# Kernel optimization log

Measured on AMD Instinct MI355X. Metric: run time of the kernel, lower is better.

Reference implementation:

```python
import jax, jax.numpy as jnp
import numpy as np

EPS = 1e-5
B, NA, T, D, H, L, DFF, E = 4, 64, 128, 128, 8, 3, 512, 65536
NN = T * NA  # nodes per graph = t*n after reshape(b, t*n, f)
DH = D // H


def _layer_norm(x, g, b):
    m = x.mean(-1, keepdims=True)
    v = ((x - m) ** 2).mean(-1, keepdims=True)
    return (x - m) * jax.lax.rsqrt(v + EPS) * g + b


def _pos_encoding(t, d):
    pos = jnp.arange(t, dtype=jnp.float32)[:, None]
    i = jnp.arange(0, d, 2, dtype=jnp.float32)
    ang = pos * jnp.exp(-jnp.log(10000.0) * i / d)
    pe = jnp.zeros((t, d), jnp.float32)
    return pe.at[:, 0::2].set(jnp.sin(ang)).at[:, 1::2].set(jnp.cos(ang))


def _forward(all_hist_feat, edge_weight, hist_w, hist_b,
             attn_wq, attn_bq, attn_wk, attn_bk, attn_wv, attn_bv, attn_wo, attn_bo,
             ln1_g, ln1_b, ff_w1, ff_b1, ff_w2, ff_b2, ln2_g, ln2_b,
             bn_g, bn_b, lin_graph_w, lin_graph_b, edge_index):
    b, n, t, _ = all_hist_feat.shape
    # history embedding: Linear(3, D)  -> [b, n, t, D]
    x = all_hist_feat @ hist_w + hist_b
    # sinusoidal positional encoding over the time axis
    out_e = x + _pos_encoding(t, D)
    scale = 1.0 / jnp.sqrt(jnp.asarray(DH, jnp.float32))
    for l in range(L):  # small fixed layer count
        q = out_e @ attn_wq[l] + attn_bq[l]
        k = out_e @ attn_wk[l] + attn_bk[l]
        v = out_e @ attn_wv[l] + attn_bv[l]
        qh = q.reshape(b, n, t, H, DH)
        kh = k.reshape(b, n, t, H, DH)
        vh = v.reshape(b, n, t, H, DH)
        scores = jnp.einsum('bnqhd,bnkhd->bnhqk', qh, kh) * scale
        attn = jax.nn.softmax(scores, axis=-1)
        o = jnp.einsum('bnhqk,bnkhd->bnqhd', attn, vh).reshape(b, n, t, D)
        o = o @ attn_wo[l] + attn_bo[l]
        h1 = _layer_norm(out_e + o, ln1_g[l], ln1_b[l])
        ff = jax.nn.relu(h1 @ ff_w1[l] + ff_b1[l]) @ ff_w2[l] + ff_b2[l]
        out_e = _layer_norm(h1 + ff, ln2_g[l], ln2_b[l])
    # graph stage: nodes are (time, agent) pairs, index = time*n + agent
    graph_w = out_e.transpose(0, 2, 1, 3).reshape(b, t * n, D)
    graph_x = x.transpose(0, 2, 1, 3).reshape(b, t * n, D)
    # GCNConv_Fixed_W (no self loops, no normalize): per-node score then
    # edge-weighted scatter-add from source to target (PyG convention)
    s = (graph_w * graph_x).sum(-1)  # [b, t*n]
    src, dst = edge_index[:, 0], edge_index[:, 1]

    def agg(s_b, src_b, dst_b, ew_b):
        return jax.ops.segment_sum(ew_b * s_b[src_b], dst_b, num_segments=NN)

    graph_out = jax.vmap(agg)(s, src, dst, edge_weight)  # [b, t*n]
    g = graph_out.reshape(b, t, n)
    # BatchNorm2d(1) on [b, 1, n, t]: single channel -> global batch stats
    m = g.mean()
    var = g.var()
    g = (g - m) * jax.lax.rsqrt(var + EPS) * bn_g[0] + bn_b[0]
    g4 = g.transpose(0, 2, 1)[..., None]  # [b, n, t, 1]
    return g4 @ lin_graph_w + lin_graph_b  # [b, n, t, D]


def setup_inputs() -> dict:
    keys = iter(jax.random.split(jax.random.key(0), 64))

    def nrm(shape, scale):
        return jax.random.normal(next(keys), shape, jnp.float32) * scale

    inp = {
        'all_hist_feat': nrm((B, NA, T, 3), 1.0),
        'edge_index': jax.random.randint(next(keys), (B, 2, E), 0, NN, jnp.int32),
        'edge_weight': jax.random.uniform(next(keys), (B, E), jnp.float32),
        'hist_w': nrm((3, D), 0.5), 'hist_b': nrm((D,), 0.02),
        'attn_wq': nrm((L, D, D), D ** -0.5), 'attn_bq': jnp.zeros((L, D)),
        'attn_wk': nrm((L, D, D), D ** -0.5), 'attn_bk': jnp.zeros((L, D)),
        'attn_wv': nrm((L, D, D), D ** -0.5), 'attn_bv': jnp.zeros((L, D)),
        'attn_wo': nrm((L, D, D), D ** -0.5), 'attn_bo': jnp.zeros((L, D)),
        'ln1_g': jnp.ones((L, D)), 'ln1_b': jnp.zeros((L, D)),
        'ff_w1': nrm((L, D, DFF), D ** -0.5), 'ff_b1': jnp.zeros((L, DFF)),
        'ff_w2': nrm((L, DFF, D), DFF ** -0.5), 'ff_b2': jnp.zeros((L, D)),
        'ln2_g': jnp.ones((L, D)), 'ln2_b': jnp.zeros((L, D)),
        'bn_g': jnp.ones((1,)), 'bn_b': jnp.zeros((1,)),
        'lin_graph_w': nrm((1, D), 1.0), 'lin_graph_b': jnp.zeros((D,)),
    }
    return inp


def reference(all_hist_feat, edge_index, edge_weight, hist_w, hist_b,
              attn_wq, attn_bq, attn_wk, attn_bk, attn_wv, attn_bv, attn_wo, attn_bo,
              ln1_g, ln1_b, ff_w1, ff_b1, ff_w2, ff_b2, ln2_g, ln2_b,
              bn_g, bn_b, lin_graph_w, lin_graph_b):
    return _forward(all_hist_feat, edge_weight, hist_w, hist_b,
                    attn_wq, attn_bq, attn_wk, attn_bk, attn_wv, attn_bv, attn_wo, attn_bo,
                    ln1_g, ln1_b, ff_w1, ff_b1, ff_w2, ff_b2, ln2_g, ln2_b,
                    bn_g, bn_b, lin_graph_w, lin_graph_b, edge_index)
```

## Files before the change

### kernel.cpp

```cpp
#include <hip/hip_runtime.h>
#include <hip/hip_bf16.h>
#include <math.h>

#define EPS_ 1e-5f
constexpr int B_ = 4, NA = 64, T_ = 128, D_ = 128, H_ = 8, L_ = 3, DFF = 512, E_ = 65536;
constexpr int DH = D_ / H_;
constexpr int NN = T_ * NA;
constexpr int NTOT = B_ * NA * T_;
constexpr int QLD = 384;
constexpr size_t NE_ = (size_t)NTOT * D_;

typedef __bf16 bf16x8 __attribute__((ext_vector_type(8)));
typedef float f32x4 __attribute__((ext_vector_type(4)));

__global__ __launch_bounds__(256) void embed_kernel(
    const float* __restrict__ hist, const float* __restrict__ w,
    const float* __restrict__ b, float* __restrict__ x, float* __restrict__ e) {
  int idx = blockIdx.x * 256 + threadIdx.x;
  if (idx >= NTOT * D_) return;
  int d = idx & (D_ - 1);
  int r = idx >> 7;
  int t = r & (T_ - 1);
  const float* hp = hist + (size_t)r * 3;
  float acc = b[d];
  acc += hp[0] * w[0 * D_ + d];
  acc += hp[1] * w[1 * D_ + d];
  acc += hp[2] * w[2 * D_ + d];
  x[idx] = acc;
  int p = d >> 1;
  float ang = (float)t * expf(-logf(10000.f) * (2.f * (float)p) / (float)D_);
  float pe = (d & 1) ? cosf(ang) : sinf(ang);
  e[idx] = acc + pe;
}

__global__ __launch_bounds__(256) void convert_weights(
    const float* __restrict__ wq, const float* __restrict__ wk,
    const float* __restrict__ wv, const float* __restrict__ wo,
    const float* __restrict__ w1, const float* __restrict__ w2,
    __bf16* __restrict__ hi, __bf16* __restrict__ lo) {
  const int LW = 196608;
  int idx = blockIdx.x * 256 + threadIdx.x;
  if (idx >= L_ * LW) return;
  int l = idx / LW;
  int rem = idx - l * LW;
  float src;
  int n, k, K, segoff;
  if (rem < 49152) {
    n = rem >> 7; k = rem & 127; K = 128; segoff = 0;
    int which = n >> 7, nl = n & 127;
    const float* W = (which == 0) ? wq : (which == 1) ? wk : wv;
    src = W[(size_t)l * 16384 + k * 128 + nl];
  } else if (rem < 65536) {
    int r2 = rem - 49152;
    n = r2 >> 7; k = r2 & 127; K = 128; segoff = 49152;
    src = wo[(size_t)l * 16384 + k * 128 + n];
  } else if (rem < 131072) {
    int r2 = rem - 65536;
    n = r2 >> 7; k = r2 & 127; K = 128; segoff = 65536;
    src = w1[(size_t)l * 65536 + k * 512 + n];
  } else {
    int r2 = rem - 131072;
    n = r2 >> 9; k = r2 & 511; K = 512; segoff = 131072;
    src = w2[(size_t)l * 65536 + k * 128 + n];
  }
  int nt = n >> 4, kt = k >> 5;
  int lane = ((k >> 3) & 3) * 16 + (n & 15);
  int j = k & 7;
  int dst = l * LW + segoff + ((nt * (K / 32) + kt) * 64 + lane) * 8 + j;
  __bf16 h = (__bf16)src;
  hi[dst] = h;
  lo[dst] = (__bf16)(src - (float)h);
}

__global__ __launch_bounds__(256) void bias_pack(
    const float* __restrict__ bq, const float* __restrict__ bk,
    const float* __restrict__ bv, float* __restrict__ pb) {
  int idx = blockIdx.x * 256 + threadIdx.x;
  if (idx >= L_ * QLD) return;
  int l = idx / QLD, n = idx - l * QLD;
  int which = n >> 7, nl = n & 127;
  const float* src = (which == 0) ? bq : (which == 1) ? bk : bv;
  pb[idx] = src[l * 128 + nl];
}

__device__ __forceinline__ void split8(const float* __restrict__ p,
                                       bf16x8& hi, bf16x8& lo) {
  float4 x0 = *(const float4*)p;
  float4 x1 = *(const float4*)(p + 4);
  float xv[8] = {x0.x, x0.y, x0.z, x0.w, x1.x, x1.y, x1.z, x1.w};
#pragma unroll
  for (int j = 0; j < 8; ++j) {
    __bf16 h = (__bf16)xv[j];
    hi[j] = h;
    lo[j] = (__bf16)(xv[j] - (float)h);
  }
}

template <int EPI, int K>
__global__ __launch_bounds__(256) void gemm_big(
    const float* __restrict__ A, int lda,
    const __bf16* __restrict__ Whi, const __bf16* __restrict__ Wlo,
    const float* __restrict__ bias,
    float* __restrict__ C, int ldc) {
  const int wave = threadIdx.x >> 6;
  const int lane = threadIdx.x & 63;
  const int m16 = lane & 15;
  const int quad = lane >> 4;
  const int wrow = wave >> 1, wcol = wave & 1;
  const int row0 = blockIdx.y * 128 + wrow * 64;
  const int col0 = blockIdx.x * 128 + wcol * 64;
  const int ctb = col0 >> 4;

  f32x4 acc[4][4] = {};
#pragma unroll
  for (int k0 = 0; k0 < K; k0 += 32) {
    bf16x8 ahi[4], alo[4];
#pragma unroll
    for (int mf = 0; mf < 4; ++mf)
      split8(A + (size_t)(row0 + mf * 16 + m16) * lda + k0 + quad * 8, ahi[mf], alo[mf]);
    bf16x8 bhi[4], blo[4];
#pragma unroll
    for (int nf = 0; nf < 4; ++nf) {
      size_t off = ((size_t)(ctb + nf) * (K / 32) + (k0 >> 5)) * 512 + lane * 8;
      bhi[nf] = *(const bf16x8*)(Whi + off);
      blo[nf] = *(const bf16x8*)(Wlo + off);
    }
#pragma unroll
    for (int mf = 0; mf < 4; ++mf)
#pragma unroll
      for (int nf = 0; nf < 4; ++nf) {
        acc[mf][nf] = __builtin_amdgcn_mfma_f32_16x16x32_bf16(ahi[mf], bhi[nf], acc[mf][nf], 0, 0, 0);
        acc[mf][nf] = __builtin_amdgcn_mfma_f32_16x16x32_bf16(ahi[mf], blo[nf], acc[mf][nf], 0, 0, 0);
        acc[mf][nf] = __builtin_amdgcn_mfma_f32_16x16x32_bf16(alo[mf], bhi[nf], acc[mf][nf], 0, 0, 0);
      }
  }
#pragma unroll
  for (int mf = 0; mf < 4; ++mf)
#pragma unroll
    for (int nf = 0; nf < 4; ++nf) {
      int c = col0 + nf * 16 + m16;
      float bj = bias[c];
#pragma unroll
      for (int reg = 0; reg < 4; ++reg) {
        int r = row0 + mf * 16 + quad * 4 + reg;
        float v = acc[mf][nf][reg] + bj;
        if (EPI == 1) v = fmaxf(v, 0.f);
        C[(size_t)r * ldc + c] = v;
      }
    }
}

template <int K>
__global__ __launch_bounds__(256) void gemm_ln(
    const float* __restrict__ A, int lda,
    const __bf16* __restrict__ Whi, const __bf16* __restrict__ Wlo,
    const float* __restrict__ bias, const float* __restrict__ resid,
    const float* __restrict__ lng, const float* __restrict__ lnb,
    float* __restrict__ C) {
  const int wave = threadIdx.x >> 6;
  const int lane = threadIdx.x & 63;
  const int m16 = lane & 15;
  const int quad = lane >> 4;
  const int wrow = wave >> 1, wcol = wave & 1;
  const int row0 = blockIdx.y * 64 + wrow * 32;
  const int col0 = wcol * 64;
  const int ctb = wcol * 4;

  f32x4 acc[2][4] = {};
#pragma unroll
  for (int k0 = 0; k0 < K; k0 += 32) {
    bf16x8 ahi[2], alo[2];
#pragma unroll
    for (int mf = 0; mf < 2; ++mf)
      split8(A + (size_t)(row0 + mf * 16 + m16) * lda + k0 + quad * 8, ahi[mf], alo[mf]);
    bf16x8 bhi[4], blo[4];
#pragma unroll
    for (int nf = 0; nf < 4; ++nf) {
      size_t off = ((size_t)(ctb + nf) * (K / 32) + (k0 >> 5)) * 512 + lane * 8;
      bhi[nf] = *(const bf16x8*)(Whi + off);
      blo[nf] = *(const bf16x8*)(Wlo + off);
    }
#pragma unroll
    for (int mf = 0; mf < 2; ++mf)
#pragma unroll
      for (int nf = 0; nf < 4; ++nf) {
        acc[mf][nf] = __builtin_amdgcn_mfma_f32_16x16x32_bf16(ahi[mf], bhi[nf], acc[mf][nf], 0, 0, 0);
        acc[mf][nf] = __builtin_amdgcn_mfma_f32_16x16x32_bf16(ahi[mf], blo[nf], acc[mf][nf], 0, 0, 0);
        acc[mf][nf] = __builtin_amdgcn_mfma_f32_16x16x32_bf16(alo[mf], bhi[nf], acc[mf][nf], 0, 0, 0);
      }
  }
  __shared__ float rs[64][2], rq[64][2];
#pragma unroll
  for (int mf = 0; mf < 2; ++mf)
#pragma unroll
    for (int reg = 0; reg < 4; ++reg) {
      int lr = wrow * 32 + mf * 16 + quad * 4 + reg;
      int gr = blockIdx.y * 64 + lr;
      float s = 0.f, qq = 0.f;
#pragma unroll
      for (int nf = 0; nf < 4; ++nf) {
        int c = col0 + nf * 16 + m16;
        float v = acc[mf][nf][reg] + bias[c] + resid[(size_t)gr * 128 + c];
        acc[mf][nf][reg] = v;
        s += v;
        qq += v * v;
      }
#pragma unroll
      for (int off = 1; off < 16; off <<= 1) {
        s += __shfl_xor(s, off, 64);
        qq += __shfl_xor(qq, off, 64);
      }
      if (m16 == 0) { rs[lr][wcol] = s; rq[lr][wcol] = qq; }
    }
  __syncthreads();
#pragma unroll
  for (int mf = 0; mf < 2; ++mf)
#pragma unroll
    for (int reg = 0; reg < 4; ++reg) {
      int lr = wrow * 32 + mf * 16 + quad * 4 + reg;
      int gr = blockIdx.y * 64 + lr;
      float mean = (rs[lr][0] + rs[lr][1]) * (1.f / 128.f);
      float var = (rq[lr][0] + rq[lr][1]) * (1.f / 128.f) - mean * mean;
      float rstd = rsqrtf(var + EPS_);
#pragma unroll
      for (int nf = 0; nf < 4; ++nf) {
        int c = col0 + nf * 16 + m16;
        C[(size_t)gr * 128 + c] = (acc[mf][nf][reg] - mean) * rstd * lng[c] + lnb[c];
      }
    }
}

template <int SDOT>
__global__ __launch_bounds__(256) void ff2_ln(
    const float* __restrict__ A,
    const __bf16* __restrict__ Whi, const __bf16* __restrict__ Wlo,
    const float* __restrict__ bias, const float* __restrict__ resid,
    const float* __restrict__ lng, const float* __restrict__ lnb,
    float* __restrict__ C,
    const float* __restrict__ bx, float* __restrict__ sdst) {
  const int wave = threadIdx.x >> 6;
  const int lane = threadIdx.x & 63;
  const int m16 = lane & 15;
  const int quad = lane >> 4;
  const int wrow = wave >> 1, wcol = wave & 1;
  const int grow0 = blockIdx.y * 64;
  const int lrow0 = wrow * 32;
  const int col0 = wcol * 64;
  const int ctb = wcol * 4;

  __shared__ float As[64][129];

  f32x4 acc[2][4] = {};
  for (int kc = 0; kc < 4; ++kc) {
    if (kc) __syncthreads();
#pragma unroll
    for (int u = 0; u < 8; ++u) {
      int unit = threadIdx.x + u * 256;
      int r = unit >> 5, c4 = unit & 31;
      float4 v = *(const float4*)(A + (size_t)(grow0 + r) * 512 + kc * 128 + c4 * 4);
      As[r][c4 * 4 + 0] = v.x;
      As[r][c4 * 4 + 1] = v.y;
      As[r][c4 * 4 + 2] = v.z;
      As[r][c4 * 4 + 3] = v.w;
    }
    __syncthreads();
#pragma unroll
    for (int kt = 0; kt < 4; ++kt) {
      bf16x8 ahi[2], alo[2];
#pragma unroll
      for (int mf = 0; mf < 2; ++mf)
        split8(&As[lrow0 + mf * 16 + m16][kt * 32 + quad * 8], ahi[mf], alo[mf]);
      bf16x8 bhi[4], blo[4];
#pragma unroll
      for (int nf = 0; nf < 4; ++nf) {
        size_t off = ((size_t)(ctb + nf) * 16 + (kc * 4 + kt)) * 512 + lane * 8;
        bhi[nf] = *(const bf16x8*)(Whi + off);
        blo[nf] = *(const bf16x8*)(Wlo + off);
      }
#pragma unroll
      for (int mf = 0; mf < 2; ++mf)
#pragma unroll
        for (int nf = 0; nf < 4; ++nf) {
          acc[mf][nf] = __builtin_amdgcn_mfma_f32_16x16x32_bf16(ahi[mf], bhi[nf], acc[mf][nf], 0, 0, 0);
          acc[mf][nf] = __builtin_amdgcn_mfma_f32_16x16x32_bf16(ahi[mf], blo[nf], acc[mf][nf], 0, 0, 0);
          acc[mf][nf] = __builtin_amdgcn_mfma_f32_16x16x32_bf16(alo[mf], bhi[nf], acc[mf][nf], 0, 0, 0);
        }
    }
  }
  __shared__ float rs[64][2], rq[64][2];
  __shared__ float sd[64][2];
#pragma unroll
  for (int mf = 0; mf < 2; ++mf)
#pragma unroll
    for (int reg = 0; reg < 4; ++reg) {
      int lr = lrow0 + mf * 16 + quad * 4 + reg;
      int gr = grow0 + lr;
      float s = 0.f, qq = 0.f;
#pragma unroll
      for (int nf = 0; nf < 4; ++nf) {
        int c = col0 + nf * 16 + m16;
        float v = acc[mf][nf][reg] + bias[c] + resid[(size_t)gr * 128 + c];
        acc[mf][nf][reg] = v;
        s += v;
        qq += v * v;
      }
#pragma unroll
      for (int off = 1; off < 16; off <<= 1) {
        s += __shfl_xor(s, off, 64);
        qq += __shfl_xor(qq, off, 64);
      }
      if (m16 == 0) { rs[lr][wcol] = s; rq[lr][wcol] = qq; }
    }
  __syncthreads();
#pragma unroll
  for (int mf = 0; mf < 2; ++mf)
#pragma unroll
    for (int reg = 0; reg < 4; ++reg) {
      int lr = lrow0 + mf * 16 + quad * 4 + reg;
      int gr = grow0 + lr;
      float mean = (rs[lr][0] + rs[lr][1]) * (1.f / 128.f);
      float var = (rq[lr][0] + rq[lr][1]) * (1.f / 128.f) - mean * mean;
      float rstd = rsqrtf(var + EPS_);
      float sdp = 0.f;
#pragma unroll
      for (int nf = 0; nf < 4; ++nf) {
        int c = col0 + nf * 16 + m16;
        float v = (acc[mf][nf][reg] - mean) * rstd * lng[c] + lnb[c];
        C[(size_t)gr * 128 + c] = v;
        if (SDOT) sdp += v * bx[(size_t)gr * 128 + c];
      }
      if (SDOT) {
#pragma unroll
        for (int off = 1; off < 16; off <<= 1) sdp += __shfl_xor(sdp, off, 64);
        if (m16 == 0) sd[lr][wcol] = sdp;
      }
    }
  if (SDOT) {
    __syncthreads();
    if (threadIdx.x < 64) {
      int lr = threadIdx.x;
      int gr = grow0 + lr;
      float sv = sd[lr][0] + sd[lr][1];
      int t = gr & (T_ - 1);
      int bn = gr >> 7;
      int n = bn & (NA - 1);
      int b = bn >> 6;
      sdst[(size_t)b * NN + t * NA + n] = sv;
    }
  }
}

__global__ __launch_bounds__(256) void attn_mfma(float* __restrict__ qkv) {
  const int h = blockIdx.x & (H_ - 1);
  const int bn = blockIdx.x >> 3;
  const int wave = threadIdx.x >> 6;
  const int lane = threadIdx.x & 63;
  const int m16 = lane & 15;
  const int quad = lane >> 4;
  const int row0 = wave * 32;
  const float* Qb = qkv + (size_t)bn * T_ * QLD + h * DH;
  const float* Kb = Qb + 128;
  const float* Vb = Qb + 256;
  float* Ob = (float*)Vb;

  __shared__ __bf16 Plds[4][32][136];
  __shared__ __bf16 KH[8][32][8], KL[8][32][8];
  __shared__ __bf16 VH[4][64][8], VL[4][64][8];

  for (int u = threadIdx.x; u < 1024; u += 256) {
    int isV = u >> 9;
    int r2 = u & 511;
    int t = r2 >> 2, c4 = r2 & 3;
    float4 v = *(const float4*)((isV ? Vb : Kb) + (size_t)t * QLD + c4 * 4);
    float xv[4] = {v.x, v.y, v.z, v.w};
#pragma unroll
    for (int i = 0; i < 4; ++i) {
      int dh = c4 * 4 + i;
      __bf16 hh = (__bf16)xv[i];
      __bf16 ll = (__bf16)(xv[i] - (float)hh);
      if (isV) {
        int kc = t >> 5, rem = t & 31;
        int vl = (rem >> 3) * 16 + dh;
        VH[kc][vl][rem & 7] = hh;
        VL[kc][vl][rem & 7] = ll;
      } else {
        int nf = t >> 4;
        int kl = (dh >> 3) * 16 + (t & 15);
        KH[nf][kl][dh & 7] = hh;
        KL[nf][kl][dh & 7] = ll;
      }
    }
  }

  bf16x8 qhi[2], qlo[2];
#pragma unroll
  for (int mf = 0; mf < 2; ++mf) {
    if (quad < 2) {
      split8(Qb + (size_t)(row0 + mf * 16 + m16) * QLD + quad * 8, qhi[mf], qlo[mf]);
    } else {
#pragma unroll
      for (int j = 0; j < 8; ++j) { qhi[mf][j] = (__bf16)0.f; qlo[mf][j] = (__bf16)0.f; }
    }
  }
  __syncthreads();

  f32x4 acc[2][8] = {};
#pragma unroll
  for (int nf = 0; nf < 8; ++nf) {
    bf16x8 khi, klo;
    if (quad < 2) {
      khi = *(const bf16x8*)&KH[nf][lane][0];
      klo = *(const bf16x8*)&KL[nf][lane][0];
    } else {
#pragma unroll
      for (int j = 0; j < 8; ++j) { khi[j] = (__bf16)0.f; klo[j] = (__bf16)0.f; }
    }
#pragma unroll
    for (int mf = 0; mf < 2; ++mf) {
      acc[mf][nf] = __builtin_amdgcn_mfma_f32_16x16x32_bf16(qhi[mf], khi, acc[mf][nf], 0, 0, 0);
      acc[mf][nf] = __builtin_amdgcn_mfma_f32_16x16x32_bf16(qhi[mf], klo, acc[mf][nf], 0, 0, 0);
      acc[mf][nf] = __builtin_amdgcn_mfma_f32_16x16x32_bf16(qlo[mf], khi, acc[mf][nf], 0, 0, 0);
    }
  }

  const float scale = 0.25f;
#pragma unroll
  for (int mf = 0; mf < 2; ++mf)
#pragma unroll
    for (int reg = 0; reg < 4; ++reg) {
      float mx = -1e30f;
#pragma unroll
      for (int nf = 0; nf < 8; ++nf) mx = fmaxf(mx, acc[mf][nf][reg]);
#pragma unroll
      for (int off = 1; off < 16; off <<= 1) mx = fmaxf(mx, __shfl_xor(mx, off, 64));
      float sum = 0.f;
#pragma unroll
      for (int nf = 0; nf < 8; ++nf) {
        float e = __expf((acc[mf][nf][reg] - mx) * scale);
        acc[mf][nf][reg] = e;
        sum += e;
      }
#pragma unroll
      for (int off = 1; off < 16; off <<= 1) sum += __shfl_xor(sum, off, 64);
      float inv = 1.f / sum;
#pragma unroll
      for (int nf = 0; nf < 8; ++nf) acc[mf][nf][reg] *= inv;
    }

#pragma unroll
  for (int mf = 0; mf < 2; ++mf)
#pragma unroll
    for (int nf = 0; nf < 8; ++nf)
#pragma unroll
      for (int reg = 0; reg < 4; ++reg)
        Plds[wave][mf * 16 + quad * 4 + reg][nf * 16 + m16] = (__bf16)acc[mf][nf][reg];

  f32x4 oacc[2] = {};
#pragma unroll
  for (int kc = 0; kc < 4; ++kc) {
    bf16x8 pa0 = *(const bf16x8*)&Plds[wave][m16][kc * 32 + quad * 8];
    bf16x8 pa1 = *(const bf16x8*)&Plds[wave][16 + m16][kc * 32 + quad * 8];
    bf16x8 vhi = *(const bf16x8*)&VH[kc][lane][0];
    bf16x8 vlo = *(const bf16x8*)&VL[kc][lane][0];
    oacc[0] = __builtin_amdgcn_mfma_f32_16x16x32_bf16(pa0, vhi, oacc[0], 0, 0, 0);
    oacc[0] = __builtin_amdgcn_mfma_f32_16x16x32_bf16(pa0, vlo, oacc[0], 0, 0, 0);
    oacc[1] = __builtin_amdgcn_mfma_f32_16x16x32_bf16(pa1, vhi, oacc[1], 0, 0, 0);
    oacc[1] = __builtin_amdgcn_mfma_f32_16x16x32_bf16(pa1, vlo, oacc[1], 0, 0, 0);
  }

#pragma unroll
  for (int mf = 0; mf < 2; ++mf)
#pragma unroll
    for (int reg = 0; reg < 4; ++reg) {
      int r = row0 + mf * 16 + quad * 4 + reg;
      Ob[(size_t)r * QLD + m16] = oacc[mf][reg];
    }
}

__global__ __launch_bounds__(256) void scatter_kernel(
    const float* __restrict__ s, const int* __restrict__ ei,
    const float* __restrict__ ew, float* __restrict__ g) {
  int idx = blockIdx.x * 256 + threadIdx.x;
  if (idx >= B_ * E_) return;
  int b = idx >> 16;
  int e = idx & (E_ - 1);
  int src = ei[(size_t)b * 2 * E_ + e];
  int dst = ei[(size_t)b * 2 * E_ + E_ + e];
  float w = ew[(size_t)b * E_ + e];
  atomicAdd(&g[(size_t)b * NN + dst], w * s[(size_t)b * NN + src]);
}

__global__ __launch_bounds__(256) void stats_partial(
    const float* __restrict__ g, float* __restrict__ st) {
  int i = blockIdx.x * 256 + threadIdx.x;
  float v = g[i];
  float sum = v, sq = v * v;
#pragma unroll
  for (int off = 32; off; off >>= 1) {
    sum += __shfl_down(sum, off, 64);
    sq += __shfl_down(sq, off, 64);
  }
  __shared__ float s1[4], s2[4];
  int w = threadIdx.x >> 6;
  if ((threadIdx.x & 63) == 0) { s1[w] = sum; s2[w] = sq; }
  __syncthreads();
  if (threadIdx.x == 0) {
    atomicAdd(&st[0], s1[0] + s1[1] + s1[2] + s1[3]);
    atomicAdd(&st[1], s2[0] + s2[1] + s2[2] + s2[3]);
  }
}

__global__ __launch_bounds__(256) void final_kernel(
    const float* __restrict__ g, const float* __restrict__ st,
    const float* __restrict__ bng, const float* __restrict__ bnb,
    const float* __restrict__ lw, const float* __restrict__ lb,
    float* __restrict__ out) {
  int idx = blockIdx.x * 256 + threadIdx.x;
  if (idx >= NTOT * D_) return;
  int d = idx & (D_ - 1);
  int r = idx >> 7;
  int t = r & (T_ - 1);
  int bn = r >> 7;
  int n = bn & (NA - 1);
  int b = bn >> 6;
  const float invn = 1.f / (float)(B_ * NN);
  float m = st[0] * invn;
  float var = st[1] * invn - m * m;
  float rs = rsqrtf(var + EPS_);
  float gv = g[(size_t)b * NN + t * NA + n];
  float val = (gv - m) * rs * bng[0] + bnb[0];
  out[idx] = val * lw[d] + lb[d];
}

extern "C" void kernel_launch(void* const* d_in, const int* in_sizes, int n_in,
                              void* d_out, int out_size, void* d_ws, size_t ws_size,
                              hipStream_t stream) {
  const float* hist = (const float*)d_in[0];
  const int* eidx = (const int*)d_in[1];
  const float* ew = (const float*)d_in[2];
  const float* hw = (const float*)d_in[3];
  const float* hb = (const float*)d_in[4];
  const float* wq = (const float*)d_in[5];
  const float* bq = (const float*)d_in[6];
  const float* wk = (const float*)d_in[7];
  const float* bk = (const float*)d_in[8];
  const float* wv = (const float*)d_in[9];
  const float* bv = (const float*)d_in[10];
  const float* wo = (const float*)d_in[11];
  const float* bo = (const float*)d_in[12];
  const float* ln1g = (const float*)d_in[13];
  const float* ln1b = (const float*)d_in[14];
  const float* w1 = (const float*)d_in[15];
  const float* b1 = (const float*)d_in[16];
  const float* w2 = (const float*)d_in[17];
  const float* b2 = (const float*)d_in[18];
  const float* ln2g = (const float*)d_in[19];
  const float* ln2b = (const float*)d_in[20];
  const float* bng = (const float*)d_in[21];
  const float* bnb = (const float*)d_in[22];
  const float* lgw = (const float*)d_in[23];
  const float* lgb = (const float*)d_in[24];
  float* out = (float*)d_out;

  float* ws = (float*)d_ws;
  const size_t NE = NE_;
  float* bx = ws + 0 * NE;
  float* be = ws + 1 * NE;
  float* h1 = ws + 2 * NE;
  float* qkv = ws + 3 * NE;
  float* ffmid = ws + 3 * NE;
  float* bs_ = ws + 7 * NE;
  float* bg_ = bs_ + NTOT;
  float* bst = bg_ + NTOT;
  float* pbias = bst + 2;
  const int LW = 196608;
  __bf16* whiB = (__bf16*)(pbias + L_ * QLD);
  __bf16* wloB = whiB + (size_t)L_ * LW;

  convert_weights<<<(L_ * LW + 255) / 256, 256, 0, stream>>>(
      wq, wk, wv, wo, w1, w2, whiB, wloB);
  bias_pack<<<(L_ * QLD + 255) / 256, 256, 0, stream>>>(bq, bk, bv, pbias);
  embed_kernel<<<(NTOT * D_) / 256, 256, 0, stream>>>(hist, hw, hb, bx, be);

  for (int l = 0; l < L_; ++l) {
    const __bf16* hiL = whiB + (size_t)l * LW;
    const __bf16* loL = wloB + (size_t)l * LW;
    gemm_big<0, 128><<<dim3(3, NTOT / 128), 256, 0, stream>>>(
        be, 128, hiL, loL, pbias + l * QLD, qkv, QLD);
    attn_mfma<<<B_ * NA * H_, 256, 0, stream>>>(qkv);
    gemm_ln<128><<<dim3(1, NTOT / 64), 256, 0, stream>>>(
        qkv + 256, QLD, hiL + 49152, loL + 49152, bo + l * D_, be,
        ln1g + l * D_, ln1b + l * D_, h1);
    gemm_big<1, 128><<<dim3(4, NTOT / 128), 256, 0, stream>>>(
        h1, 128, hiL + 65536, loL + 65536, b1 + l * DFF, ffmid, 512);
    if (l < L_ - 1) {
      ff2_ln<0><<<dim3(1, NTOT / 64), 256, 0, stream>>>(
          ffmid, hiL + 131072, loL + 131072, b2 + l * D_, h1,
          ln2g + l * D_, ln2b + l * D_, be, nullptr, nullptr);
    } else {
      ff2_ln<1><<<dim3(1, NTOT / 64), 256, 0, stream>>>(
          ffmid, hiL + 131072, loL + 131072, b2 + l * D_, h1,
          ln2g + l * D_, ln2b + l * D_, be, bx, bs_);
    }
  }

  hipMemsetAsync(bg_, 0, ((size_t)B_ * NN + 2) * sizeof(float), stream);
  scatter_kernel<<<(B_ * E_) / 256, 256, 0, stream>>>(bs_, eidx, ew, bg_);
  stats_partial<<<(B_ * NN) / 256, 256, 0, stream>>>(bg_, bst);
  final_kernel<<<(NTOT * D_) / 256, 256, 0, stream>>>(bg_, bst, bng, bnb, lgw, lgb, out);
}
```

Measured before the change: 538.9 us.

## Fuse FFN up-projection, ReLU and down-projection+LayerNorm into one kernel

```diff
diff --git a/kernel.cpp b/kernel.cpp
--- a/kernel.cpp
+++ b/kernel.cpp
@@ -231,76 +231,93 @@
 }
 
 template <int SDOT>
-__global__ __launch_bounds__(256) void ff2_ln(
+__global__ __launch_bounds__(256) void ff_fused(
     const float* __restrict__ A,
-    const __bf16* __restrict__ Whi, const __bf16* __restrict__ Wlo,
-    const float* __restrict__ bias, const float* __restrict__ resid,
+    const __bf16* __restrict__ W1hi, const __bf16* __restrict__ W1lo,
+    const float* __restrict__ b1v,
+    const __bf16* __restrict__ W2hi, const __bf16* __restrict__ W2lo,
+    const float* __restrict__ b2v, const float* __restrict__ resid,
     const float* __restrict__ lng, const float* __restrict__ lnb,
     float* __restrict__ C,
     const float* __restrict__ bx, float* __restrict__ sdst) {
+  extern __shared__ float Amid[];
   const int wave = threadIdx.x >> 6;
   const int lane = threadIdx.x & 63;
   const int m16 = lane & 15;
   const int quad = lane >> 4;
-  const int wrow = wave >> 1, wcol = wave & 1;
-  const int grow0 = blockIdx.y * 64;
-  const int lrow0 = wrow * 32;
-  const int col0 = wcol * 64;
-  const int ctb = wcol * 4;
-
-  __shared__ float As[64][129];
-
-  f32x4 acc[2][4] = {};
-  for (int kc = 0; kc < 4; ++kc) {
-    if (kc) __syncthreads();
-#pragma unroll
-    for (int u = 0; u < 8; ++u) {
-      int unit = threadIdx.x + u * 256;
-      int r = unit >> 5, c4 = unit & 31;
-      float4 v = *(const float4*)(A + (size_t)(grow0 + r) * 512 + kc * 128 + c4 * 4);
-      As[r][c4 * 4 + 0] = v.x;
-      As[r][c4 * 4 + 1] = v.y;
-      As[r][c4 * 4 + 2] = v.z;
-      As[r][c4 * 4 + 3] = v.w;
-    }
-    __syncthreads();
+  const int grow0 = blockIdx.x * 32;
+
+  {
+    f32x4 acc[2][8] = {};
 #pragma unroll
     for (int kt = 0; kt < 4; ++kt) {
       bf16x8 ahi[2], alo[2];
 #pragma unroll
       for (int mf = 0; mf < 2; ++mf)
-        split8(&As[lrow0 + mf * 16 + m16][kt * 32 + quad * 8], ahi[mf], alo[mf]);
-      bf16x8 bhi[4], blo[4];
-#pragma unroll
-      for (int nf = 0; nf < 4; ++nf) {
-        size_t off = ((size_t)(ctb + nf) * 16 + (kc * 4 + kt)) * 512 + lane * 8;
-        bhi[nf] = *(const bf16x8*)(Whi + off);
-        blo[nf] = *(const bf16x8*)(Wlo + off);
-      }
-#pragma unroll
-      for (int mf = 0; mf < 2; ++mf)
-#pragma unroll
-        for (int nf = 0; nf < 4; ++nf) {
-          acc[mf][nf] = __builtin_amdgcn_mfma_f32_16x16x32_bf16(ahi[mf], bhi[nf], acc[mf][nf], 0, 0, 0);
-          acc[mf][nf] = __builtin_amdgcn_mfma_f32_16x16x32_bf16(ahi[mf], blo[nf], acc[mf][nf], 0, 0, 0);
-          acc[mf][nf] = __builtin_amdgcn_mfma_f32_16x16x32_bf16(alo[mf], bhi[nf], acc[mf][nf], 0, 0, 0);
+        split8(A + (size_t)(grow0 + mf * 16 + m16) * 128 + kt * 32 + quad * 8, ahi[mf], alo[mf]);
+#pragma unroll
+      for (int nf = 0; nf < 8; ++nf) {
+        size_t off = ((size_t)(wave * 8 + nf) * 4 + kt) * 512 + lane * 8;
+        bf16x8 bhi = *(const bf16x8*)(W1hi + off);
+        bf16x8 blo = *(const bf16x8*)(W1lo + off);
+#pragma unroll
+        for (int mf = 0; mf < 2; ++mf) {
+          acc[mf][nf] = __builtin_amdgcn_mfma_f32_16x16x32_bf16(ahi[mf], bhi, acc[mf][nf], 0, 0, 0);
+          acc[mf][nf] = __builtin_amdgcn_mfma_f32_16x16x32_bf16(ahi[mf], blo, acc[mf][nf], 0, 0, 0);
+          acc[mf][nf] = __builtin_amdgcn_mfma_f32_16x16x32_bf16(alo[mf], bhi, acc[mf][nf], 0, 0, 0);
         }
-    }
-  }
-  __shared__ float rs[64][2], rq[64][2];
-  __shared__ float sd[64][2];
+      }
+    }
+#pragma unroll
+    for (int mf = 0; mf < 2; ++mf)
+#pragma unroll
+      for (int nf = 0; nf < 8; ++nf) {
+        int c = wave * 128 + nf * 16 + m16;
+        float bj = b1v[c];
+#pragma unroll
+        for (int reg = 0; reg < 4; ++reg) {
+          int r = mf * 16 + quad * 4 + reg;
+          Amid[r * 513 + c] = fmaxf(acc[mf][nf][reg] + bj, 0.f);
+        }
+      }
+  }
+  __syncthreads();
+
+  f32x4 acc2[2][2] = {};
+#pragma unroll
+  for (int kt = 0; kt < 16; ++kt) {
+    bf16x8 ahi[2], alo[2];
+#pragma unroll
+    for (int mf = 0; mf < 2; ++mf)
+      split8(&Amid[(mf * 16 + m16) * 513 + kt * 32 + quad * 8], ahi[mf], alo[mf]);
+#pragma unroll
+    for (int nf = 0; nf < 2; ++nf) {
+      size_t off = ((size_t)(wave * 2 + nf) * 16 + kt) * 512 + lane * 8;
+      bf16x8 bhi = *(const bf16x8*)(W2hi + off);
+      bf16x8 blo = *(const bf16x8*)(W2lo + off);
+#pragma unroll
+      for (int mf = 0; mf < 2; ++mf) {
+        acc2[mf][nf] = __builtin_amdgcn_mfma_f32_16x16x32_bf16(ahi[mf], bhi, acc2[mf][nf], 0, 0, 0);
+        acc2[mf][nf] = __builtin_amdgcn_mfma_f32_16x16x32_bf16(ahi[mf], blo, acc2[mf][nf], 0, 0, 0);
+        acc2[mf][nf] = __builtin_amdgcn_mfma_f32_16x16x32_bf16(alo[mf], bhi, acc2[mf][nf], 0, 0, 0);
+      }
+    }
+  }
+
+  __shared__ float rs[32][4], rq[32][4], sd[32][4];
+  const int col0 = wave * 32;
 #pragma unroll
   for (int mf = 0; mf < 2; ++mf)
 #pragma unroll
     for (int reg = 0; reg < 4; ++reg) {
-      int lr = lrow0 + mf * 16 + quad * 4 + reg;
+      int lr = mf * 16 + quad * 4 + reg;
       int gr = grow0 + lr;
       float s = 0.f, qq = 0.f;
 #pragma unroll
-      for (int nf = 0; nf < 4; ++nf) {
+      for (int nf = 0; nf < 2; ++nf) {
         int c = col0 + nf * 16 + m16;
-        float v = acc[mf][nf][reg] + bias[c] + resid[(size_t)gr * 128 + c];
-        acc[mf][nf][reg] = v;
+        float v = acc2[mf][nf][reg] + b2v[c] + resid[(size_t)gr * 128 + c];
+        acc2[mf][nf][reg] = v;
         s += v;
         qq += v * v;
       }
@@ -309,38 +326,38 @@
         s += __shfl_xor(s, off, 64);
         qq += __shfl_xor(qq, off, 64);
       }
-      if (m16 == 0) { rs[lr][wcol] = s; rq[lr][wcol] = qq; }
+      if (m16 == 0) { rs[lr][wave] = s; rq[lr][wave] = qq; }
     }
   __syncthreads();
 #pragma unroll
   for (int mf = 0; mf < 2; ++mf)
 #pragma unroll
     for (int reg = 0; reg < 4; ++reg) {
-      int lr = lrow0 + mf * 16 + quad * 4 + reg;
+      int lr = mf * 16 + quad * 4 + reg;
       int gr = grow0 + lr;
-      float mean = (rs[lr][0] + rs[lr][1]) * (1.f / 128.f);
-      float var = (rq[lr][0] + rq[lr][1]) * (1.f / 128.f) - mean * mean;
+      float mean = (rs[lr][0] + rs[lr][1] + rs[lr][2] + rs[lr][3]) * (1.f / 128.f);
+      float var = (rq[lr][0] + rq[lr][1] + rq[lr][2] + rq[lr][3]) * (1.f / 128.f) - mean * mean;
       float rstd = rsqrtf(var + EPS_);
       float sdp = 0.f;
 #pragma unroll
-      for (int nf = 0; nf < 4; ++nf) {
+      for (int nf = 0; nf < 2; ++nf) {
         int c = col0 + nf * 16 + m16;
-        float v = (acc[mf][nf][reg] - mean) * rstd * lng[c] + lnb[c];
+        float v = (acc2[mf][nf][reg] - mean) * rstd * lng[c] + lnb[c];
         C[(size_t)gr * 128 + c] = v;
         if (SDOT) sdp += v * bx[(size_t)gr * 128 + c];
       }
       if (SDOT) {
 #pragma unroll
         for (int off = 1; off < 16; off <<= 1) sdp += __shfl_xor(sdp, off, 64);
-        if (m16 == 0) sd[lr][wcol] = sdp;
+        if (m16 == 0) sd[lr][wave] = sdp;
       }
     }
   if (SDOT) {
     __syncthreads();
-    if (threadIdx.x < 64) {
+    if (threadIdx.x < 32) {
       int lr = threadIdx.x;
       int gr = grow0 + lr;
-      float sv = sd[lr][0] + sd[lr][1];
+      float sv = sd[lr][0] + sd[lr][1] + sd[lr][2] + sd[lr][3];
       int t = gr & (T_ - 1);
       int bn = gr >> 7;
       int n = bn & (NA - 1);
@@ -568,7 +585,6 @@
   float* be = ws + 1 * NE;
   float* h1 = ws + 2 * NE;
   float* qkv = ws + 3 * NE;
-  float* ffmid = ws + 3 * NE;
   float* bs_ = ws + 7 * NE;
   float* bg_ = bs_ + NTOT;
   float* bst = bg_ + NTOT;
@@ -576,6 +592,16 @@
   const int LW = 196608;
   __bf16* whiB = (__bf16*)(pbias + L_ * QLD);
   __bf16* wloB = whiB + (size_t)L_ * LW;
+
+  const size_t ffshm = (size_t)32 * 513 * sizeof(float);
+  static bool ff_attr_done = false;
+  if (!ff_attr_done) {
+    (void)hipFuncSetAttribute(reinterpret_cast<const void*>(&ff_fused<0>),
+                              hipFuncAttributeMaxDynamicSharedMemorySize, (int)ffshm);
+    (void)hipFuncSetAttribute(reinterpret_cast<const void*>(&ff_fused<1>),
+                              hipFuncAttributeMaxDynamicSharedMemorySize, (int)ffshm);
+    ff_attr_done = true;
+  }
 
   convert_weights<<<(L_ * LW + 255) / 256, 256, 0, stream>>>(
       wq, wk, wv, wo, w1, w2, whiB, wloB);
@@ -591,15 +617,15 @@
     gemm_ln<128><<<dim3(1, NTOT / 64), 256, 0, stream>>>(
         qkv + 256, QLD, hiL + 49152, loL + 49152, bo + l * D_, be,
         ln1g + l * D_, ln1b + l * D_, h1);
-    gemm_big<1, 128><<<dim3(4, NTOT / 128), 256, 0, stream>>>(
-        h1, 128, hiL + 65536, loL + 65536, b1 + l * DFF, ffmid, 512);
     if (l < L_ - 1) {
-      ff2_ln<0><<<dim3(1, NTOT / 64), 256, 0, stream>>>(
-          ffmid, hiL + 131072, loL + 131072, b2 + l * D_, h1,
+      ff_fused<0><<<NTOT / 32, 256, ffshm, stream>>>(
+          h1, hiL + 65536, loL + 65536, b1 + l * DFF,
+          hiL + 131072, loL + 131072, b2 + l * D_, h1,
           ln2g + l * D_, ln2b + l * D_, be, nullptr, nullptr);
     } else {
-      ff2_ln<1><<<dim3(1, NTOT / 64), 256, 0, stream>>>(
-          ffmid, hiL + 131072, loL + 131072, b2 + l * D_, h1,
+      ff_fused<1><<<NTOT / 32, 256, ffshm, stream>>>(
+          h1, hiL + 65536, loL + 65536, b1 + l * DFF,
+          hiL + 131072, loL + 131072, b2 + l * D_, h1,
           ln2g + l * D_, ln2b + l * D_, be, bx, bs_);
     }
   }
```

New measurement: 547.3 us. About the same (+1.6%).

## Fuse QKV projection into attention kernel per (batch,agent,head) block

Applied to the files above, without the earlier changes.

```diff
diff --git a/kernel.cpp b/kernel.cpp
--- a/kernel.cpp
+++ b/kernel.cpp
@@ -350,7 +350,11 @@
   }
 }
 
-__global__ __launch_bounds__(256) void attn_mfma(float* __restrict__ qkv) {
+__global__ __launch_bounds__(256) void attn_fused(
+    const float* __restrict__ A,
+    const __bf16* __restrict__ Whi, const __bf16* __restrict__ Wlo,
+    const float* __restrict__ pb,
+    float* __restrict__ O) {
   const int h = blockIdx.x & (H_ - 1);
   const int bn = blockIdx.x >> 3;
   const int wave = threadIdx.x >> 6;
@@ -358,45 +362,78 @@
   const int m16 = lane & 15;
   const int quad = lane >> 4;
   const int row0 = wave * 32;
-  const float* Qb = qkv + (size_t)bn * T_ * QLD + h * DH;
-  const float* Kb = Qb + 128;
-  const float* Vb = Qb + 256;
-  float* Ob = (float*)Vb;
+  const float* Ab = A + (size_t)bn * T_ * 128;
 
   __shared__ __bf16 Plds[4][32][136];
   __shared__ __bf16 KH[8][32][8], KL[8][32][8];
   __shared__ __bf16 VH[4][64][8], VL[4][64][8];
-
-  for (int u = threadIdx.x; u < 1024; u += 256) {
-    int isV = u >> 9;
-    int r2 = u & 511;
-    int t = r2 >> 2, c4 = r2 & 3;
-    float4 v = *(const float4*)((isV ? Vb : Kb) + (size_t)t * QLD + c4 * 4);
-    float xv[4] = {v.x, v.y, v.z, v.w};
-#pragma unroll
-    for (int i = 0; i < 4; ++i) {
-      int dh = c4 * 4 + i;
-      __bf16 hh = (__bf16)xv[i];
-      __bf16 ll = (__bf16)(xv[i] - (float)hh);
-      if (isV) {
+  __bf16* QHw = &Plds[wave][0][0];
+  __bf16* QLw = QHw + 512;
+
+  f32x4 qkv[2][3] = {};
+#pragma unroll
+  for (int k0 = 0; k0 < 128; k0 += 32) {
+    bf16x8 ahi[2], alo[2];
+#pragma unroll
+    for (int mf = 0; mf < 2; ++mf)
+      split8(Ab + (size_t)(row0 + mf * 16 + m16) * 128 + k0 + quad * 8, ahi[mf], alo[mf]);
+    bf16x8 bhi[3], blo[3];
+#pragma unroll
+    for (int s = 0; s < 3; ++s) {
+      size_t off = ((size_t)(s * 8 + h) * 4 + (k0 >> 5)) * 512 + lane * 8;
+      bhi[s] = *(const bf16x8*)(Whi + off);
+      blo[s] = *(const bf16x8*)(Wlo + off);
+    }
+#pragma unroll
+    for (int mf = 0; mf < 2; ++mf)
+#pragma unroll
+      for (int s = 0; s < 3; ++s) {
+        qkv[mf][s] = __builtin_amdgcn_mfma_f32_16x16x32_bf16(ahi[mf], bhi[s], qkv[mf][s], 0, 0, 0);
+        qkv[mf][s] = __builtin_amdgcn_mfma_f32_16x16x32_bf16(ahi[mf], blo[s], qkv[mf][s], 0, 0, 0);
+        qkv[mf][s] = __builtin_amdgcn_mfma_f32_16x16x32_bf16(alo[mf], bhi[s], qkv[mf][s], 0, 0, 0);
+      }
+  }
+
+#pragma unroll
+  for (int mf = 0; mf < 2; ++mf)
+#pragma unroll
+    for (int reg = 0; reg < 4; ++reg) {
+      const int tl = mf * 16 + quad * 4 + reg;
+      const int t = row0 + tl;
+      const int dh = m16;
+      {
+        float v = qkv[mf][0][reg] + pb[h * 16 + dh];
+        __bf16 hh = (__bf16)v;
+        __bf16 ll = (__bf16)(v - (float)hh);
+        int idx = mf * 256 + ((dh >> 3) * 16 + (tl & 15)) * 8 + (dh & 7);
+        QHw[idx] = hh;
+        QLw[idx] = ll;
+      }
+      {
+        float v = qkv[mf][1][reg] + pb[128 + h * 16 + dh];
+        __bf16 hh = (__bf16)v;
+        __bf16 ll = (__bf16)(v - (float)hh);
+        KH[t >> 4][(dh >> 3) * 16 + (t & 15)][dh & 7] = hh;
+        KL[t >> 4][(dh >> 3) * 16 + (t & 15)][dh & 7] = ll;
+      }
+      {
+        float v = qkv[mf][2][reg] + pb[256 + h * 16 + dh];
+        __bf16 hh = (__bf16)v;
+        __bf16 ll = (__bf16)(v - (float)hh);
         int kc = t >> 5, rem = t & 31;
         int vl = (rem >> 3) * 16 + dh;
         VH[kc][vl][rem & 7] = hh;
         VL[kc][vl][rem & 7] = ll;
-      } else {
-        int nf = t >> 4;
-        int kl = (dh >> 3) * 16 + (t & 15);
-        KH[nf][kl][dh & 7] = hh;
-        KL[nf][kl][dh & 7] = ll;
-      }
-    }
-  }
+      }
+    }
 
   bf16x8 qhi[2], qlo[2];
 #pragma unroll
   for (int mf = 0; mf < 2; ++mf) {
     if (quad < 2) {
-      split8(Qb + (size_t)(row0 + mf * 16 + m16) * QLD + quad * 8, qhi[mf], qlo[mf]);
+      int idx = mf * 256 + (quad * 16 + m16) * 8;
+      qhi[mf] = *(const bf16x8*)&QHw[idx];
+      qlo[mf] = *(const bf16x8*)&QLw[idx];
     } else {
 #pragma unroll
       for (int j = 0; j < 8; ++j) { qhi[mf][j] = (__bf16)0.f; qlo[mf][j] = (__bf16)0.f; }
@@ -473,7 +510,7 @@
 #pragma unroll
     for (int reg = 0; reg < 4; ++reg) {
       int r = row0 + mf * 16 + quad * 4 + reg;
-      Ob[(size_t)r * QLD + m16] = oacc[mf][reg];
+      O[((size_t)bn * T_ + r) * 128 + h * 16 + m16] = oacc[mf][reg];
     }
 }
 
@@ -567,7 +604,7 @@
   float* bx = ws + 0 * NE;
   float* be = ws + 1 * NE;
   float* h1 = ws + 2 * NE;
-  float* qkv = ws + 3 * NE;
+  float* obuf = ws + 3 * NE;
   float* ffmid = ws + 3 * NE;
   float* bs_ = ws + 7 * NE;
   float* bg_ = bs_ + NTOT;
@@ -585,11 +622,10 @@
   for (int l = 0; l < L_; ++l) {
     const __bf16* hiL = whiB + (size_t)l * LW;
     const __bf16* loL = wloB + (size_t)l * LW;
-    gemm_big<0, 128><<<dim3(3, NTOT / 128), 256, 0, stream>>>(
-        be, 128, hiL, loL, pbias + l * QLD, qkv, QLD);
-    attn_mfma<<<B_ * NA * H_, 256, 0, stream>>>(qkv);
+    attn_fused<<<B_ * NA * H_, 256, 0, stream>>>(
+        be, hiL, loL, pbias + l * QLD, obuf);
     gemm_ln<128><<<dim3(1, NTOT / 64), 256, 0, stream>>>(
-        qkv + 256, QLD, hiL + 49152, loL + 49152, bo + l * D_, be,
+        obuf, 128, hiL + 49152, loL + 49152, bo + l * D_, be,
         ln1g + l * D_, ln1b + l * D_, h1);
     gemm_big<1, 128><<<dim3(4, NTOT / 128), 256, 0, stream>>>(
         h1, 128, hiL + 65536, loL + 65536, b1 + l * DFF, ffmid, 512);
```

Measured after the change: 505.0 us. -6.3%, faster.
